# Performance work log

Measured on AMD Instinct MI355X. Metric: run time of the kernel, lower is better.

## Reference

```python
import jax, jax.numpy as jnp
import numpy as np

N = 100000
E = 1600000
F_IN = 128
F_OUT = 128
BN_EPS = 1e-5


def setup_inputs() -> dict:
    key = jax.random.key(0)
    ks = jax.random.split(key, 8)
    x = jax.random.normal(ks[0], (N, F_IN), dtype=jnp.float32)
    edge_index = jax.random.randint(ks[1], (2, E), 0, N, dtype=jnp.int64)
    s1 = 1.0 / np.sqrt(F_IN)
    s2 = 1.0 / np.sqrt(F_OUT)
    W1 = jax.random.uniform(ks[2], (F_OUT, F_IN), jnp.float32, -s1, s1)
    b1 = jax.random.uniform(ks[3], (F_OUT,), jnp.float32, -s1, s1)
    gamma = jnp.ones((F_OUT,), jnp.float32)
    beta = jnp.zeros((F_OUT,), jnp.float32)
    W2 = jax.random.uniform(ks[4], (F_OUT, F_OUT), jnp.float32, -s2, s2)
    b2 = jax.random.uniform(ks[5], (F_OUT,), jnp.float32, -s2, s2)
    eps = jnp.zeros((1,), jnp.float32)
    return {"x": x, "edge_index": edge_index, "eps": eps, "W1": W1, "b1": b1,
            "gamma": gamma, "beta": beta, "W2": W2, "b2": b2}


def reference(x, edge_index, eps, W1, b1, gamma, beta, W2, b2):
    row, col = edge_index[0], edge_index[1]
    # gather neighbor features then scatter-add by destination node
    neighbor_sum = jax.ops.segment_sum(x[col], row, num_segments=x.shape[0])
    out = (1.0 + eps) * x + neighbor_sum  # [N, F_IN]
    h = out @ W1.T + b1                   # [N, F_OUT]
    # BatchNorm1d in training mode: biased batch statistics over nodes
    mean = jnp.mean(h, axis=0)
    var = jnp.mean(jnp.square(h - mean), axis=0)
    h = (h - mean) * jax.lax.rsqrt(var + BN_EPS) * gamma + beta
    h = jax.nn.relu(h)
    return h @ W2.T + b2
```

## Files before the change

kernel.cpp:

```cpp
#include <hip/hip_runtime.h>
#include <hip/hip_bf16.h>

#define NF 128

typedef __attribute__((ext_vector_type(8))) short short8;
typedef __attribute__((ext_vector_type(4))) float f32x4;

__device__ __forceinline__ ushort f2bf(float f) {
    union { __hip_bfloat16 h; ushort u; } c;
    c.h = __float2bfloat16(f);
    return c.u;
}
__device__ __forceinline__ float bf_lo(uint u) { return __uint_as_float(u << 16); }
__device__ __forceinline__ float bf_hi(uint u) { return __uint_as_float(u & 0xffff0000u); }

#define EPB 4096

__global__ void cvt_hist_kernel(const float* __restrict__ x, const float* __restrict__ W1,
                                const float* __restrict__ W2, ushort* __restrict__ xb,
                                ushort* __restrict__ W1b, ushort* __restrict__ W2b,
                                const int* __restrict__ ei, int* __restrict__ binCnt,
                                int nx4, int nblkC, int E) {
    __shared__ int lcnt[256];
    int t = threadIdx.x;
    int blk = blockIdx.x;
    if (blk < nblkC) {
        lcnt[t] = 0;
        __syncthreads();
        int base = blk * EPB;
#pragma unroll
        for (int it = 0; it < EPB / 256; it++) {
            int e = base + it * 256 + t;
            if (e < E) atomicAdd(&lcnt[ei[e] >> 9], 1);
        }
        __syncthreads();
        int c = lcnt[t];
        if (c) atomicAdd(&binCnt[t], c);
    }
    int gid = blk * 256 + t;
    const float* src;
    ushort* dst;
    int idx;
    if (gid < nx4) { src = x; dst = xb; idx = gid; }
    else if (gid < nx4 + 4096) { src = W1; dst = W1b; idx = gid - nx4; }
    else if (gid < nx4 + 8192) { src = W2; dst = W2b; idx = gid - nx4 - 4096; }
    else return;
    float4 v = reinterpret_cast<const float4*>(src)[idx];
    ushort4 o;
    o.x = f2bf(v.x); o.y = f2bf(v.y); o.z = f2bf(v.z); o.w = f2bf(v.w);
    reinterpret_cast<ushort4*>(dst)[idx] = o;
}

__global__ void passC_kernel(const int* __restrict__ ei, const int* __restrict__ binCnt,
                             int* __restrict__ binOff, uint2* __restrict__ pair, int E) {
    __shared__ uint2 sorted[EPB];
    __shared__ int lcnt[256];
    __shared__ int lofs[256];
    __shared__ int scanB[256];
    __shared__ int lcur[256];
    __shared__ int gdelta[256];
    int t = threadIdx.x;
    lcnt[t] = 0;
    lcur[t] = 0;
    __syncthreads();
    int base = blockIdx.x * EPB;
    int rows[EPB / 256], cols[EPB / 256];
#pragma unroll
    for (int it = 0; it < EPB / 256; it++) {
        int e = base + it * 256 + t;
        rows[it] = (e < E) ? ei[e] : -1;
        cols[it] = (e < E) ? ei[E + e] : 0;
        if (rows[it] >= 0) atomicAdd(&lcnt[rows[it] >> 9], 1);
    }
    __syncthreads();
    int v = lcnt[t];
    lofs[t] = v;
    int bc = binCnt[t];
    scanB[t] = bc;
    __syncthreads();
#pragma unroll
    for (int off = 1; off < 256; off <<= 1) {
        int u1 = (t >= off) ? lofs[t - off] : 0;
        int u2 = (t >= off) ? scanB[t - off] : 0;
        __syncthreads();
        lofs[t] += u1;
        scanB[t] += u2;
        __syncthreads();
    }
    int myOfs = lofs[t] - v;
    int binBase_t = scanB[t] - bc;
    int g = v ? atomicAdd(&binOff[t], v) : 0;
    __syncthreads();
    lofs[t] = myOfs;
    gdelta[t] = binBase_t + g - myOfs;
    __syncthreads();
#pragma unroll
    for (int it = 0; it < EPB / 256; it++) {
        if (rows[it] >= 0) {
            int b = rows[it] >> 9;
            int p = lofs[b] + atomicAdd(&lcur[b], 1);
            sorted[p] = make_uint2((uint)rows[it], (uint)cols[it]);
        }
    }
    __syncthreads();
    int nvalid = min(EPB, E - base);
    for (int i = t; i < nvalid; i += 256) {
        uint2 pr = sorted[i];
        pair[gdelta[pr.x >> 9] + i] = pr;
    }
}

__global__ void passDE_kernel(const uint2* __restrict__ pair, const int* __restrict__ binCnt,
                              int* __restrict__ rowptr, int* __restrict__ adj, int N, int E) {
    __shared__ int hist[512];
    __shared__ int s2[256];
    __shared__ int cur[512];
    int t = threadIdx.x;
    int b = blockIdx.x;
    hist[t] = 0;
    hist[t + 256] = 0;
    s2[t] = (t < b) ? binCnt[t] : 0;
    __syncthreads();
#pragma unroll
    for (int off = 128; off > 0; off >>= 1) {
        if (t < off) s2[t] += s2[t + off];
        __syncthreads();
    }
    int base = s2[0];
    int cnt = binCnt[b];
    __syncthreads();
    for (int i = t; i < cnt; i += 256)
        atomicAdd(&hist[pair[base + i].x & 511], 1);
    __syncthreads();
    int h0 = hist[2 * t], h1 = hist[2 * t + 1];
    s2[t] = h0 + h1;
    __syncthreads();
#pragma unroll
    for (int off = 1; off < 256; off <<= 1) {
        int u = (t >= off) ? s2[t - off] : 0;
        __syncthreads();
        s2[t] += u;
        __syncthreads();
    }
    int e0 = base + s2[t] - (h0 + h1);
    int e1 = e0 + h0;
    int g0 = b * 512 + 2 * t;
    if (g0 < N) rowptr[g0] = e0;
    if (g0 + 1 < N) rowptr[g0 + 1] = e1;
    if (t == 0 && b == gridDim.x - 1) rowptr[N] = E;
    cur[2 * t] = e0;
    cur[2 * t + 1] = e1;
    __syncthreads();
    for (int i = t; i < cnt; i += 256) {
        uint2 p = pair[base + i];
        int slot = atomicAdd(&cur[p.x & 511], 1);
        adj[slot] = (int)p.y;
    }
}

#define ACCV(v)                                                   \
    a0 += bf_lo((v).x); a1 += bf_hi((v).x);                       \
    a2 += bf_lo((v).y); a3 += bf_hi((v).y);                       \
    a4 += bf_lo((v).z); a5 += bf_hi((v).z);                       \
    a6 += bf_lo((v).w); a7 += bf_hi((v).w);

__global__ void gather_kernel(const uint4* __restrict__ xb4, const int* __restrict__ rowptr,
                              const int* __restrict__ adj, const float* __restrict__ eps,
                              uint4* __restrict__ aggb4, int N) {
    int t = blockIdx.x * blockDim.x + threadIdx.x;
    int node = t >> 4;
    int lane = t & 15;
    if (node >= N) return;
    uint4 u = xb4[(size_t)node * 16 + lane];
    float s = 1.0f + eps[0];
    float a0 = bf_lo(u.x) * s, a1 = bf_hi(u.x) * s;
    float a2 = bf_lo(u.y) * s, a3 = bf_hi(u.y) * s;
    float a4 = bf_lo(u.z) * s, a5 = bf_hi(u.z) * s;
    float a6 = bf_lo(u.w) * s, a7 = bf_hi(u.w) * s;
    int j = rowptr[node], end = rowptr[node + 1];
    for (; j + 8 <= end; j += 8) {
        int c0 = adj[j],     c1 = adj[j + 1], c2 = adj[j + 2], c3 = adj[j + 3];
        int c4 = adj[j + 4], c5 = adj[j + 5], c6 = adj[j + 6], c7 = adj[j + 7];
        uint4 v0 = xb4[(size_t)c0 * 16 + lane];
        uint4 v1 = xb4[(size_t)c1 * 16 + lane];
        uint4 v2 = xb4[(size_t)c2 * 16 + lane];
        uint4 v3 = xb4[(size_t)c3 * 16 + lane];
        uint4 v4 = xb4[(size_t)c4 * 16 + lane];
        uint4 v5 = xb4[(size_t)c5 * 16 + lane];
        uint4 v6 = xb4[(size_t)c6 * 16 + lane];
        uint4 v7 = xb4[(size_t)c7 * 16 + lane];
        ACCV(v0) ACCV(v1) ACCV(v2) ACCV(v3)
        ACCV(v4) ACCV(v5) ACCV(v6) ACCV(v7)
    }
    if (j + 4 <= end) {
        int c0 = adj[j], c1 = adj[j + 1], c2 = adj[j + 2], c3 = adj[j + 3];
        uint4 v0 = xb4[(size_t)c0 * 16 + lane];
        uint4 v1 = xb4[(size_t)c1 * 16 + lane];
        uint4 v2 = xb4[(size_t)c2 * 16 + lane];
        uint4 v3 = xb4[(size_t)c3 * 16 + lane];
        ACCV(v0) ACCV(v1) ACCV(v2) ACCV(v3)
        j += 4;
    }
    if (j + 2 <= end) {
        int c0 = adj[j], c1 = adj[j + 1];
        uint4 v0 = xb4[(size_t)c0 * 16 + lane];
        uint4 v1 = xb4[(size_t)c1 * 16 + lane];
        ACCV(v0) ACCV(v1)
        j += 2;
    }
    if (j < end) {
        uint4 v0 = xb4[(size_t)adj[j] * 16 + lane];
        ACCV(v0)
    }
    uint4 o;
    o.x = (uint)f2bf(a0) | ((uint)f2bf(a1) << 16);
    o.y = (uint)f2bf(a2) | ((uint)f2bf(a3) << 16);
    o.z = (uint)f2bf(a4) | ((uint)f2bf(a5) << 16);
    o.w = (uint)f2bf(a6) | ((uint)f2bf(a7) << 16);
    aggb4[(size_t)node * 16 + lane] = o;
}

template <int MODE>
__global__ __launch_bounds__(256) void mgemm_kernel(
    const ushort* __restrict__ Ab, const ushort* __restrict__ Wb,
    const float* __restrict__ bias, float* __restrict__ out,
    ushort* __restrict__ hb, float* __restrict__ stats,
    const float* __restrict__ gamma, const float* __restrict__ beta, int N) {
    __shared__ ushort As[128 * 136];
    __shared__ ushort Bs[128 * 136];
    __shared__ float redS[256];
    __shared__ float redQ[256];
    __shared__ float scL[128];
    __shared__ float shL[128];

    const int t = threadIdx.x;
    const int row0 = blockIdx.x * 128;
    const int r16 = t >> 4;
    const int c8 = (t & 15) * 8;

    if (MODE == 1 && t < 128) {
        float inv_n = 1.0f / (float)N;
        float mean = stats[t] * inv_n;
        float var = fmaxf(stats[128 + t] * inv_n - mean * mean, 0.0f);
        float s = gamma[t] * rsqrtf(var + 1e-5f);
        scL[t] = s;
        shL[t] = beta[t] - mean * s;
    }
    if (MODE == 1) __syncthreads();

    float sc[8], sh[8];
    if (MODE == 1) {
#pragma unroll
        for (int i = 0; i < 8; i++) { sc[i] = scL[c8 + i]; sh[i] = shL[c8 + i]; }
    }

#pragma unroll
    for (int it = 0; it < 8; it++) {
        int row = it * 16 + r16;
        int gr = row0 + row;
        if (MODE == 0) {
            uint4 v = make_uint4(0, 0, 0, 0);
            if (gr < N) v = *reinterpret_cast<const uint4*>(Ab + (size_t)gr * NF + c8);
            *reinterpret_cast<uint4*>(&As[row * 136 + c8]) = v;
        } else {
            uint4 v = make_uint4(0, 0, 0, 0);
            if (gr < N) v = *reinterpret_cast<const uint4*>(hb + (size_t)gr * NF + c8);
            float vv[8] = {bf_lo(v.x), bf_hi(v.x), bf_lo(v.y), bf_hi(v.y),
                           bf_lo(v.z), bf_hi(v.z), bf_lo(v.w), bf_hi(v.w)};
#pragma unroll
            for (int i = 0; i < 8; i++) vv[i] = fmaxf(vv[i] * sc[i] + sh[i], 0.0f);
            uint4 p;
            p.x = (uint)f2bf(vv[0]) | ((uint)f2bf(vv[1]) << 16);
            p.y = (uint)f2bf(vv[2]) | ((uint)f2bf(vv[3]) << 16);
            p.z = (uint)f2bf(vv[4]) | ((uint)f2bf(vv[5]) << 16);
            p.w = (uint)f2bf(vv[6]) | ((uint)f2bf(vv[7]) << 16);
            *reinterpret_cast<uint4*>(&As[row * 136 + c8]) = p;
        }
        uint4 w = *reinterpret_cast<const uint4*>(Wb + row * NF + c8);
        *reinterpret_cast<uint4*>(&Bs[row * 136 + c8]) = w;
    }
    __syncthreads();

    const int wid = t >> 6;
    const int lane = t & 63;
    const int quad = lane >> 4;
    const int l16 = lane & 15;
    const int wm = wid >> 1;
    const int wn = wid & 1;

    f32x4 acc[4][4];
#pragma unroll
    for (int tm = 0; tm < 4; tm++)
#pragma unroll
        for (int tn = 0; tn < 4; tn++) acc[tm][tn] = (f32x4)(0.0f);

#pragma unroll
    for (int ks = 0; ks < 4; ks++) {
        short8 a[4], b[4];
#pragma unroll
        for (int tm = 0; tm < 4; tm++)
            a[tm] = *reinterpret_cast<const short8*>(
                &As[(wm * 64 + tm * 16 + l16) * 136 + ks * 32 + quad * 8]);
#pragma unroll
        for (int tn = 0; tn < 4; tn++)
            b[tn] = *reinterpret_cast<const short8*>(
                &Bs[(wn * 64 + tn * 16 + l16) * 136 + ks * 32 + quad * 8]);
#pragma unroll
        for (int tm = 0; tm < 4; tm++)
#pragma unroll
            for (int tn = 0; tn < 4; tn++)
                acc[tm][tn] = __builtin_amdgcn_mfma_f32_16x16x32_bf16(a[tm], b[tn],
                                                                      acc[tm][tn], 0, 0, 0);
    }

    float bs[4];
#pragma unroll
    for (int tn = 0; tn < 4; tn++) bs[tn] = bias[wn * 64 + tn * 16 + l16];

    float ssum[4] = {0.f, 0.f, 0.f, 0.f}, sq[4] = {0.f, 0.f, 0.f, 0.f};
#pragma unroll
    for (int tm = 0; tm < 4; tm++) {
        int rb = wm * 64 + tm * 16 + quad * 4;
#pragma unroll
        for (int reg = 0; reg < 4; reg++) {
            int gr = row0 + rb + reg;
            bool ok = gr < N;
#pragma unroll
            for (int tn = 0; tn < 4; tn++) {
                int col = wn * 64 + tn * 16 + l16;
                float h = acc[tm][tn][reg] + bs[tn];
                if (ok) {
                    if (MODE == 0) {
                        hb[(size_t)gr * NF + col] = f2bf(h);
                        ssum[tn] += h;
                        sq[tn] += h * h;
                    } else {
                        out[(size_t)gr * NF + col] = h;
                    }
                }
            }
        }
    }

    if (MODE == 0) {
#pragma unroll
        for (int tn = 0; tn < 4; tn++) {
            float s = ssum[tn], q = sq[tn];
            s += __shfl_xor(s, 16); s += __shfl_xor(s, 32);
            q += __shfl_xor(q, 16); q += __shfl_xor(q, 32);
            if (quad == 0) {
                int c = wn * 64 + tn * 16 + l16;
                redS[wm * 128 + c] = s;
                redQ[wm * 128 + c] = q;
            }
        }
        __syncthreads();
        if (t < 128) {
            unsafeAtomicAdd(&stats[t], redS[t] + redS[128 + t]);
            unsafeAtomicAdd(&stats[128 + t], redQ[t] + redQ[128 + t]);
        }
    }
}

extern "C" void kernel_launch(void* const* d_in, const int* in_sizes, int n_in,
                              void* d_out, int out_size, void* d_ws, size_t ws_size,
                              hipStream_t stream) {
    const float* x     = (const float*)d_in[0];
    const int* ei      = (const int*)d_in[1];
    const float* eps   = (const float*)d_in[2];
    const float* W1    = (const float*)d_in[3];
    const float* b1    = (const float*)d_in[4];
    const float* gamma = (const float*)d_in[5];
    const float* beta  = (const float*)d_in[6];
    const float* W2    = (const float*)d_in[7];
    const float* b2    = (const float*)d_in[8];
    float* out         = (float*)d_out;

    const int N = in_sizes[0] / NF;
    const int E = in_sizes[1] / 2;

    const int NB = (N + 511) >> 9;
    const int nblkC = (E + EPB - 1) / EPB;

    ushort* xb     = (ushort*)d_ws;
    ushort* aggb   = xb + (size_t)N * NF;
    ushort* W1b    = aggb + (size_t)N * NF;
    ushort* W2b    = W1b + NF * NF;
    float*  stats  = (float*)(W2b + NF * NF);
    int*    binCnt = (int*)(stats + 512);
    int*    binOff = binCnt + 256;
    int*    rowptr = binOff + 256;
    int*    adj    = rowptr + (N + 1);
    uint2*  pair   = (uint2*)aggb;
    ushort* hb     = xb;

    hipMemsetAsync(stats, 0, 4096, stream);

    int nx4 = N * 32;
    int cvtBlocks = (nx4 + 8192 + 255) / 256;
    cvt_hist_kernel<<<cvtBlocks, 256, 0, stream>>>(x, W1, W2, xb, W1b, W2b, ei, binCnt,
                                                   nx4, nblkC, E);
    passC_kernel<<<nblkC, 256, 0, stream>>>(ei, binCnt, binOff, pair, E);
    passDE_kernel<<<NB, 256, 0, stream>>>(pair, binCnt, rowptr, adj, N, E);

    long long gt = (long long)N * 16;
    gather_kernel<<<(int)((gt + 255) / 256), 256, 0, stream>>>((const uint4*)xb, rowptr, adj,
                                                               eps, (uint4*)aggb, N);

    int gblocks = (N + 127) / 128;
    mgemm_kernel<0><<<gblocks, 256, 0, stream>>>(aggb, W1b, b1, out, hb, stats,
                                                 nullptr, nullptr, N);
    mgemm_kernel<1><<<gblocks, 256, 0, stream>>>(nullptr, W2b, b2, out, hb, stats,
                                                 gamma, beta, N);
}
```

Measured before the change: 278.0 us.

## Fuse neighbor gather-aggregation into first GEMM kernel

Removes the standalone gather kernel and performs the CSR neighbor aggregation directly into the shared-memory A tile of the first GEMM. This avoids writing and re-reading the aggregated bf16 feature matrix through global memory and saves a launch. In exchange, the latency-bound random gathers now run inside a large-LDS GEMM block with lower occupancy and a serial per-row loop, which may reduce memory-level parallelism.

```diff
diff --git a/kernel.cpp b/kernel.cpp
--- a/kernel.cpp
+++ b/kernel.cpp
@@ -164,72 +164,168 @@
     a4 += bf_lo((v).z); a5 += bf_hi((v).z);                       \
     a6 += bf_lo((v).w); a7 += bf_hi((v).w);
 
-__global__ void gather_kernel(const uint4* __restrict__ xb4, const int* __restrict__ rowptr,
-                              const int* __restrict__ adj, const float* __restrict__ eps,
-                              uint4* __restrict__ aggb4, int N) {
-    int t = blockIdx.x * blockDim.x + threadIdx.x;
-    int node = t >> 4;
-    int lane = t & 15;
-    if (node >= N) return;
-    uint4 u = xb4[(size_t)node * 16 + lane];
-    float s = 1.0f + eps[0];
-    float a0 = bf_lo(u.x) * s, a1 = bf_hi(u.x) * s;
-    float a2 = bf_lo(u.y) * s, a3 = bf_hi(u.y) * s;
-    float a4 = bf_lo(u.z) * s, a5 = bf_hi(u.z) * s;
-    float a6 = bf_lo(u.w) * s, a7 = bf_hi(u.w) * s;
-    int j = rowptr[node], end = rowptr[node + 1];
-    for (; j + 8 <= end; j += 8) {
-        int c0 = adj[j],     c1 = adj[j + 1], c2 = adj[j + 2], c3 = adj[j + 3];
-        int c4 = adj[j + 4], c5 = adj[j + 5], c6 = adj[j + 6], c7 = adj[j + 7];
-        uint4 v0 = xb4[(size_t)c0 * 16 + lane];
-        uint4 v1 = xb4[(size_t)c1 * 16 + lane];
-        uint4 v2 = xb4[(size_t)c2 * 16 + lane];
-        uint4 v3 = xb4[(size_t)c3 * 16 + lane];
-        uint4 v4 = xb4[(size_t)c4 * 16 + lane];
-        uint4 v5 = xb4[(size_t)c5 * 16 + lane];
-        uint4 v6 = xb4[(size_t)c6 * 16 + lane];
-        uint4 v7 = xb4[(size_t)c7 * 16 + lane];
-        ACCV(v0) ACCV(v1) ACCV(v2) ACCV(v3)
-        ACCV(v4) ACCV(v5) ACCV(v6) ACCV(v7)
-    }
-    if (j + 4 <= end) {
-        int c0 = adj[j], c1 = adj[j + 1], c2 = adj[j + 2], c3 = adj[j + 3];
-        uint4 v0 = xb4[(size_t)c0 * 16 + lane];
-        uint4 v1 = xb4[(size_t)c1 * 16 + lane];
-        uint4 v2 = xb4[(size_t)c2 * 16 + lane];
-        uint4 v3 = xb4[(size_t)c3 * 16 + lane];
-        ACCV(v0) ACCV(v1) ACCV(v2) ACCV(v3)
-        j += 4;
-    }
-    if (j + 2 <= end) {
-        int c0 = adj[j], c1 = adj[j + 1];
-        uint4 v0 = xb4[(size_t)c0 * 16 + lane];
-        uint4 v1 = xb4[(size_t)c1 * 16 + lane];
-        ACCV(v0) ACCV(v1)
-        j += 2;
-    }
-    if (j < end) {
-        uint4 v0 = xb4[(size_t)adj[j] * 16 + lane];
-        ACCV(v0)
-    }
-    uint4 o;
-    o.x = (uint)f2bf(a0) | ((uint)f2bf(a1) << 16);
-    o.y = (uint)f2bf(a2) | ((uint)f2bf(a3) << 16);
-    o.z = (uint)f2bf(a4) | ((uint)f2bf(a5) << 16);
-    o.w = (uint)f2bf(a6) | ((uint)f2bf(a7) << 16);
-    aggb4[(size_t)node * 16 + lane] = o;
-}
-
-template <int MODE>
-__global__ __launch_bounds__(256) void mgemm_kernel(
-    const ushort* __restrict__ Ab, const ushort* __restrict__ Wb,
-    const float* __restrict__ bias, float* __restrict__ out,
-    ushort* __restrict__ hb, float* __restrict__ stats,
-    const float* __restrict__ gamma, const float* __restrict__ beta, int N) {
+__global__ __launch_bounds__(256) void mgemm0_fused(
+    const uint4* __restrict__ xb4, const int* __restrict__ rowptr,
+    const int* __restrict__ adj, const float* __restrict__ eps,
+    const ushort* __restrict__ Wb, const float* __restrict__ bias,
+    ushort* __restrict__ hb, float* __restrict__ stats, int N) {
     __shared__ ushort As[128 * 136];
     __shared__ ushort Bs[128 * 136];
     __shared__ float redS[256];
     __shared__ float redQ[256];
+
+    const int t = threadIdx.x;
+    const int row0 = blockIdx.x * 128;
+    const int r16 = t >> 4;
+    const int l16i = t & 15;
+
+#pragma unroll
+    for (int it = 0; it < 8; it++) {
+        int row = it * 16 + r16;
+        uint4 w = *reinterpret_cast<const uint4*>(Wb + row * NF + l16i * 8);
+        *reinterpret_cast<uint4*>(&Bs[row * 136 + l16i * 8]) = w;
+    }
+
+    float s = 1.0f + eps[0];
+#pragma unroll 1
+    for (int it = 0; it < 8; it++) {
+        int row = it * 16 + r16;
+        int node = row0 + row;
+        float a0 = 0.f, a1 = 0.f, a2 = 0.f, a3 = 0.f;
+        float a4 = 0.f, a5 = 0.f, a6 = 0.f, a7 = 0.f;
+        if (node < N) {
+            uint4 u = xb4[(size_t)node * 16 + l16i];
+            a0 = bf_lo(u.x) * s; a1 = bf_hi(u.x) * s;
+            a2 = bf_lo(u.y) * s; a3 = bf_hi(u.y) * s;
+            a4 = bf_lo(u.z) * s; a5 = bf_hi(u.z) * s;
+            a6 = bf_lo(u.w) * s; a7 = bf_hi(u.w) * s;
+            int j = rowptr[node], end = rowptr[node + 1];
+            for (; j + 8 <= end; j += 8) {
+                int c0 = adj[j],     c1 = adj[j + 1], c2 = adj[j + 2], c3 = adj[j + 3];
+                int c4 = adj[j + 4], c5 = adj[j + 5], c6 = adj[j + 6], c7 = adj[j + 7];
+                uint4 v0 = xb4[(size_t)c0 * 16 + l16i];
+                uint4 v1 = xb4[(size_t)c1 * 16 + l16i];
+                uint4 v2 = xb4[(size_t)c2 * 16 + l16i];
+                uint4 v3 = xb4[(size_t)c3 * 16 + l16i];
+                uint4 v4 = xb4[(size_t)c4 * 16 + l16i];
+                uint4 v5 = xb4[(size_t)c5 * 16 + l16i];
+                uint4 v6 = xb4[(size_t)c6 * 16 + l16i];
+                uint4 v7 = xb4[(size_t)c7 * 16 + l16i];
+                ACCV(v0) ACCV(v1) ACCV(v2) ACCV(v3)
+                ACCV(v4) ACCV(v5) ACCV(v6) ACCV(v7)
+            }
+            if (j + 4 <= end) {
+                int c0 = adj[j], c1 = adj[j + 1], c2 = adj[j + 2], c3 = adj[j + 3];
+                uint4 v0 = xb4[(size_t)c0 * 16 + l16i];
+                uint4 v1 = xb4[(size_t)c1 * 16 + l16i];
+                uint4 v2 = xb4[(size_t)c2 * 16 + l16i];
+                uint4 v3 = xb4[(size_t)c3 * 16 + l16i];
+                ACCV(v0) ACCV(v1) ACCV(v2) ACCV(v3)
+                j += 4;
+            }
+            if (j + 2 <= end) {
+                int c0 = adj[j], c1 = adj[j + 1];
+                uint4 v0 = xb4[(size_t)c0 * 16 + l16i];
+                uint4 v1 = xb4[(size_t)c1 * 16 + l16i];
+                ACCV(v0) ACCV(v1)
+                j += 2;
+            }
+            if (j < end) {
+                uint4 v0 = xb4[(size_t)adj[j] * 16 + l16i];
+                ACCV(v0)
+            }
+        }
+        uint4 o;
+        o.x = (uint)f2bf(a0) | ((uint)f2bf(a1) << 16);
+        o.y = (uint)f2bf(a2) | ((uint)f2bf(a3) << 16);
+        o.z = (uint)f2bf(a4) | ((uint)f2bf(a5) << 16);
+        o.w = (uint)f2bf(a6) | ((uint)f2bf(a7) << 16);
+        *reinterpret_cast<uint4*>(&As[row * 136 + l16i * 8]) = o;
+    }
+    __syncthreads();
+
+    const int wid = t >> 6;
+    const int lane = t & 63;
+    const int quad = lane >> 4;
+    const int l16 = lane & 15;
+    const int wm = wid >> 1;
+    const int wn = wid & 1;
+
+    f32x4 acc[4][4];
+#pragma unroll
+    for (int tm = 0; tm < 4; tm++)
+#pragma unroll
+        for (int tn = 0; tn < 4; tn++) acc[tm][tn] = (f32x4)(0.0f);
+
+#pragma unroll
+    for (int ks = 0; ks < 4; ks++) {
+        short8 a[4], b[4];
+#pragma unroll
+        for (int tm = 0; tm < 4; tm++)
+            a[tm] = *reinterpret_cast<const short8*>(
+                &As[(wm * 64 + tm * 16 + l16) * 136 + ks * 32 + quad * 8]);
+#pragma unroll
+        for (int tn = 0; tn < 4; tn++)
+            b[tn] = *reinterpret_cast<const short8*>(
+                &Bs[(wn * 64 + tn * 16 + l16) * 136 + ks * 32 + quad * 8]);
+#pragma unroll
+        for (int tm = 0; tm < 4; tm++)
+#pragma unroll
+            for (int tn = 0; tn < 4; tn++)
+                acc[tm][tn] = __builtin_amdgcn_mfma_f32_16x16x32_bf16(a[tm], b[tn],
+                                                                      acc[tm][tn], 0, 0, 0);
+    }
+
+    float bs[4];
+#pragma unroll
+    for (int tn = 0; tn < 4; tn++) bs[tn] = bias[wn * 64 + tn * 16 + l16];
+
+    float ssum[4] = {0.f, 0.f, 0.f, 0.f}, sq[4] = {0.f, 0.f, 0.f, 0.f};
+#pragma unroll
+    for (int tm = 0; tm < 4; tm++) {
+        int rb = wm * 64 + tm * 16 + quad * 4;
+#pragma unroll
+        for (int reg = 0; reg < 4; reg++) {
+            int gr = row0 + rb + reg;
+            bool ok = gr < N;
+#pragma unroll
+            for (int tn = 0; tn < 4; tn++) {
+                int col = wn * 64 + tn * 16 + l16;
+                float h = acc[tm][tn][reg] + bs[tn];
+                if (ok) {
+                    hb[(size_t)gr * NF + col] = f2bf(h);
+                    ssum[tn] += h;
+                    sq[tn] += h * h;
+                }
+            }
+        }
+    }
+
+#pragma unroll
+    for (int tn = 0; tn < 4; tn++) {
+        float sv = ssum[tn], q = sq[tn];
+        sv += __shfl_xor(sv, 16); sv += __shfl_xor(sv, 32);
+        q += __shfl_xor(q, 16); q += __shfl_xor(q, 32);
+        if (quad == 0) {
+            int c = wn * 64 + tn * 16 + l16;
+            redS[wm * 128 + c] = sv;
+            redQ[wm * 128 + c] = q;
+        }
+    }
+    __syncthreads();
+    if (t < 128) {
+        unsafeAtomicAdd(&stats[t], redS[t] + redS[128 + t]);
+        unsafeAtomicAdd(&stats[128 + t], redQ[t] + redQ[128 + t]);
+    }
+}
+
+__global__ __launch_bounds__(256) void mgemm1_kernel(
+    const ushort* __restrict__ hb, const ushort* __restrict__ Wb,
+    const float* __restrict__ bias, float* __restrict__ out,
+    const float* __restrict__ stats, const float* __restrict__ gamma,
+    const float* __restrict__ beta, int N) {
+    __shared__ ushort As[128 * 136];
+    __shared__ ushort Bs[128 * 136];
     __shared__ float scL[128];
     __shared__ float shL[128];
 
@@ -238,7 +334,7 @@
     const int r16 = t >> 4;
     const int c8 = (t & 15) * 8;
 
-    if (MODE == 1 && t < 128) {
+    if (t < 128) {
         float inv_n = 1.0f / (float)N;
         float mean = stats[t] * inv_n;
         float var = fmaxf(stats[128 + t] * inv_n - mean * mean, 0.0f);
@@ -246,36 +342,28 @@
         scL[t] = s;
         shL[t] = beta[t] - mean * s;
     }
-    if (MODE == 1) __syncthreads();
+    __syncthreads();
 
     float sc[8], sh[8];
-    if (MODE == 1) {
-#pragma unroll
-        for (int i = 0; i < 8; i++) { sc[i] = scL[c8 + i]; sh[i] = shL[c8 + i]; }
-    }
+#pragma unroll
+    for (int i = 0; i < 8; i++) { sc[i] = scL[c8 + i]; sh[i] = shL[c8 + i]; }
 
 #pragma unroll
     for (int it = 0; it < 8; it++) {
         int row = it * 16 + r16;
         int gr = row0 + row;
-        if (MODE == 0) {
-            uint4 v = make_uint4(0, 0, 0, 0);
-            if (gr < N) v = *reinterpret_cast<const uint4*>(Ab + (size_t)gr * NF + c8);
-            *reinterpret_cast<uint4*>(&As[row * 136 + c8]) = v;
-        } else {
-            uint4 v = make_uint4(0, 0, 0, 0);
-            if (gr < N) v = *reinterpret_cast<const uint4*>(hb + (size_t)gr * NF + c8);
-            float vv[8] = {bf_lo(v.x), bf_hi(v.x), bf_lo(v.y), bf_hi(v.y),
-                           bf_lo(v.z), bf_hi(v.z), bf_lo(v.w), bf_hi(v.w)};
-#pragma unroll
-            for (int i = 0; i < 8; i++) vv[i] = fmaxf(vv[i] * sc[i] + sh[i], 0.0f);
-            uint4 p;
-            p.x = (uint)f2bf(vv[0]) | ((uint)f2bf(vv[1]) << 16);
-            p.y = (uint)f2bf(vv[2]) | ((uint)f2bf(vv[3]) << 16);
-            p.z = (uint)f2bf(vv[4]) | ((uint)f2bf(vv[5]) << 16);
-            p.w = (uint)f2bf(vv[6]) | ((uint)f2bf(vv[7]) << 16);
-            *reinterpret_cast<uint4*>(&As[row * 136 + c8]) = p;
-        }
+        uint4 v = make_uint4(0, 0, 0, 0);
+        if (gr < N) v = *reinterpret_cast<const uint4*>(hb + (size_t)gr * NF + c8);
+        float vv[8] = {bf_lo(v.x), bf_hi(v.x), bf_lo(v.y), bf_hi(v.y),
+                       bf_lo(v.z), bf_hi(v.z), bf_lo(v.w), bf_hi(v.w)};
+#pragma unroll
+        for (int i = 0; i < 8; i++) vv[i] = fmaxf(vv[i] * sc[i] + sh[i], 0.0f);
+        uint4 p;
+        p.x = (uint)f2bf(vv[0]) | ((uint)f2bf(vv[1]) << 16);
+        p.y = (uint)f2bf(vv[2]) | ((uint)f2bf(vv[3]) << 16);
+        p.z = (uint)f2bf(vv[4]) | ((uint)f2bf(vv[5]) << 16);
+        p.w = (uint)f2bf(vv[6]) | ((uint)f2bf(vv[7]) << 16);
+        *reinterpret_cast<uint4*>(&As[row * 136 + c8]) = p;
         uint4 w = *reinterpret_cast<const uint4*>(Wb + row * NF + c8);
         *reinterpret_cast<uint4*>(&Bs[row * 136 + c8]) = w;
     }
@@ -317,47 +405,19 @@
 #pragma unroll
     for (int tn = 0; tn < 4; tn++) bs[tn] = bias[wn * 64 + tn * 16 + l16];
 
-    float ssum[4] = {0.f, 0.f, 0.f, 0.f}, sq[4] = {0.f, 0.f, 0.f, 0.f};
 #pragma unroll
     for (int tm = 0; tm < 4; tm++) {
         int rb = wm * 64 + tm * 16 + quad * 4;
 #pragma unroll
         for (int reg = 0; reg < 4; reg++) {
             int gr = row0 + rb + reg;
-            bool ok = gr < N;
-#pragma unroll
-            for (int tn = 0; tn < 4; tn++) {
-                int col = wn * 64 + tn * 16 + l16;
-                float h = acc[tm][tn][reg] + bs[tn];
-                if (ok) {
-                    if (MODE == 0) {
-                        hb[(size_t)gr * NF + col] = f2bf(h);
-                        ssum[tn] += h;
-                        sq[tn] += h * h;
-                    } else {
-                        out[(size_t)gr * NF + col] = h;
-                    }
+            if (gr < N) {
+#pragma unroll
+                for (int tn = 0; tn < 4; tn++) {
+                    int col = wn * 64 + tn * 16 + l16;
+                    out[(size_t)gr * NF + col] = acc[tm][tn][reg] + bs[tn];
                 }
             }
-        }
-    }
-
-    if (MODE == 0) {
-#pragma unroll
-        for (int tn = 0; tn < 4; tn++) {
-            float s = ssum[tn], q = sq[tn];
-            s += __shfl_xor(s, 16); s += __shfl_xor(s, 32);
-            q += __shfl_xor(q, 16); q += __shfl_xor(q, 32);
-            if (quad == 0) {
-                int c = wn * 64 + tn * 16 + l16;
-                redS[wm * 128 + c] = s;
-                redQ[wm * 128 + c] = q;
-            }
-        }
-        __syncthreads();
-        if (t < 128) {
-            unsafeAtomicAdd(&stats[t], redS[t] + redS[128 + t]);
-            unsafeAtomicAdd(&stats[128 + t], redQ[t] + redQ[128 + t]);
         }
     }
 }
@@ -383,16 +443,15 @@
     const int nblkC = (E + EPB - 1) / EPB;
 
     ushort* xb     = (ushort*)d_ws;
-    ushort* aggb   = xb + (size_t)N * NF;
-    ushort* W1b    = aggb + (size_t)N * NF;
+    ushort* hb     = xb + (size_t)N * NF;
+    ushort* W1b    = hb + (size_t)N * NF;
     ushort* W2b    = W1b + NF * NF;
     float*  stats  = (float*)(W2b + NF * NF);
     int*    binCnt = (int*)(stats + 512);
     int*    binOff = binCnt + 256;
     int*    rowptr = binOff + 256;
     int*    adj    = rowptr + (N + 1);
-    uint2*  pair   = (uint2*)aggb;
-    ushort* hb     = xb;
+    uint2*  pair   = (uint2*)hb;
 
     hipMemsetAsync(stats, 0, 4096, stream);
 
@@ -403,13 +462,8 @@
     passC_kernel<<<nblkC, 256, 0, stream>>>(ei, binCnt, binOff, pair, E);
     passDE_kernel<<<NB, 256, 0, stream>>>(pair, binCnt, rowptr, adj, N, E);
 
-    long long gt = (long long)N * 16;
-    gather_kernel<<<(int)((gt + 255) / 256), 256, 0, stream>>>((const uint4*)xb, rowptr, adj,
-                                                               eps, (uint4*)aggb, N);
-
     int gblocks = (N + 127) / 128;
-    mgemm_kernel<0><<<gblocks, 256, 0, stream>>>(aggb, W1b, b1, out, hb, stats,
-                                                 nullptr, nullptr, N);
-    mgemm_kernel<1><<<gblocks, 256, 0, stream>>>(nullptr, W2b, b2, out, hb, stats,
-                                                 gamma, beta, N);
-}
+    mgemm0_fused<<<gblocks, 256, 0, stream>>>((const uint4*)xb, rowptr, adj, eps,
+                                              W1b, b1, hb, stats, N);
+    mgemm1_kernel<<<gblocks, 256, 0, stream>>>(hb, W2b, b2, out, stats, gamma, beta, N);
+}
```

New measurement: 285.0 us. +2.5%, slower.
